# Kernel tuning notes

Measured on AMD Instinct MI355X. Metric: run time of the kernel, lower is better.

Reference implementation:

```python
import jax, jax.numpy as jnp
import numpy as np

INPUT_SIZE = 64
HIDDEN_SIZE = 128
LATENT_B = 8
BATCH = 512
SEQ = 2048


def setup_inputs() -> dict:
    key = jax.random.key(0)
    ks = jax.random.split(key, 8)
    s_fc = 1.0 / np.sqrt(INPUT_SIZE)
    s_gru = 1.0 / np.sqrt(LATENT_B)
    return {
        "latent_A_seq": jax.random.normal(ks[0], (BATCH, SEQ, INPUT_SIZE), dtype=jnp.float32),
        # fc_in: Linear(input_size -> hidden_size)
        "W_in": jax.random.uniform(ks[1], (HIDDEN_SIZE, INPUT_SIZE), jnp.float32, -s_fc, s_fc),
        "b_in": jax.random.uniform(ks[2], (HIDDEN_SIZE,), jnp.float32, -s_fc, s_fc),
        # GRU(hidden_size -> latent_dim_B), PyTorch layout: [3*H, in] stacked as (r, z, n)
        "W_ih": jax.random.uniform(ks[3], (3 * LATENT_B, HIDDEN_SIZE), jnp.float32, -s_gru, s_gru),
        "W_hh": jax.random.uniform(ks[4], (3 * LATENT_B, LATENT_B), jnp.float32, -s_gru, s_gru),
        "b_ih": jax.random.uniform(ks[5], (3 * LATENT_B,), jnp.float32, -s_gru, s_gru),
        "b_hh": jax.random.uniform(ks[6], (3 * LATENT_B,), jnp.float32, -s_gru, s_gru),
    }


def reference(latent_A_seq, W_in, b_in, W_ih, W_hh, b_ih, b_hh):
    # fc_in projection: (B, S, input) -> (B, S, hidden)
    x = jnp.einsum("bsi,hi->bsh", latent_A_seq, W_in) + b_in
    H = W_hh.shape[1]

    # Precompute input-side gate activations for all timesteps: (B, S, 3H)
    x_gates = jnp.einsum("bsh,gh->bsg", x, W_ih) + b_ih
    xr, xz, xn = jnp.split(x_gates, 3, axis=-1)

    Whr, Whz, Whn = jnp.split(W_hh, 3, axis=0)
    bhr, bhz, bhn = jnp.split(b_hh, 3, axis=0)

    def step(h, gates_t):
        xr_t, xz_t, xn_t = gates_t
        r = jax.nn.sigmoid(xr_t + h @ Whr.T + bhr)
        z = jax.nn.sigmoid(xz_t + h @ Whz.T + bhz)
        n = jnp.tanh(xn_t + r * (h @ Whn.T + bhn))
        h_new = (1.0 - z) * n + z * h
        return h_new, None

    h0 = jnp.zeros((latent_A_seq.shape[0], H), dtype=latent_A_seq.dtype)
    # scan over time: move seq axis to front -> (S, B, H) per gate
    seq_gates = (jnp.swapaxes(xr, 0, 1), jnp.swapaxes(xz, 0, 1), jnp.swapaxes(xn, 0, 1))
    h_final, _ = jax.lax.scan(step, h0, seq_gates)
    return h_final  # (B, latent_dim_B) == h_n.squeeze(0)
```

## Files before the change

### kernel.cpp

```cpp
#include <hip/hip_runtime.h>
#include <math.h>

#define BATCH  512
#define SEQ    2048
#define INPUT  64
#define HID    128
#define LB     8
#define NG     24
#define GSTRIDE (BATCH * NG)
#define T      16
#define NCHUNK (SEQ / T)
#define SLABF  (LB * NG)
#define CH_F   (T * SLABF)

__global__ void precompute_kernel(const float* __restrict__ W_in,
                                  const float* __restrict__ b_in,
                                  const float* __restrict__ W_ih,
                                  const float* __restrict__ b_ih,
                                  const float* __restrict__ b_hh,
                                  float* __restrict__ Wc,
                                  float* __restrict__ bc)
{
    int t = blockIdx.x * blockDim.x + threadIdx.x;
    if (t < NG * INPUT) {
        int g = t / INPUT, i = t % INPUT;
        float acc = 0.f;
        for (int h = 0; h < HID; ++h)
            acc += W_ih[g * HID + h] * W_in[h * INPUT + i];
        Wc[t] = acc;
    } else if (t < NG * INPUT + NG) {
        int g = t - NG * INPUT;
        float acc = b_ih[g];
        if (g < 2 * LB) acc += b_hh[g];
        for (int h = 0; h < HID; ++h)
            acc += W_ih[g * HID + h] * b_in[h];
        bc[g] = acc;
    }
}

#define TS 16
#define TB 8

__global__ __launch_bounds__(128) void gates_kernel(
    const float* __restrict__ A,
    const float* __restrict__ Wc,
    const float* __restrict__ bc,
    float* __restrict__ gates)
{
    const int s0 = blockIdx.x * TS;
    const int b0 = blockIdx.y * TB;
    const int tid = threadIdx.x;

    __shared__ float sA[TB * TS * 68];

#pragma unroll
    for (int it = 0; it < 16; ++it) {
        int f    = it * 128 + tid;
        int beta = f >> 8;
        int rem  = f & 255;
        int srow = rem >> 4;
        int c4   = rem & 15;
        float4 v = *(const float4*)(A + ((size_t)(b0 + beta) * SEQ + s0 + srow) * INPUT + c4 * 4);
        *(float4*)(&sA[(beta * TS + srow) * 68 + c4 * 4]) = v;
    }
    __syncthreads();

    const int bh = tid & 7;
    const int sh = tid >> 3;
    const float4* row4 = (const float4*)(&sA[(bh * TS + sh) * 68]);
    const float4* Wc4  = (const float4*)Wc;

    float acc[NG];
#pragma unroll
    for (int g = 0; g < NG; ++g) acc[g] = bc[g];

#pragma unroll
    for (int i = 0; i < 16; ++i) {
        float4 a = row4[i];
#pragma unroll
        for (int g = 0; g < NG; ++g) {
            float4 w = Wc4[g * 16 + i];
            acc[g] += a.x * w.x + a.y * w.y + a.z * w.z + a.w * w.w;
        }
    }

    float o[NG];
#pragma unroll
    for (int j = 0; j < LB; ++j) {
        o[j * 3 + 0] = acc[j];
        o[j * 3 + 1] = acc[8 + j];
        o[j * 3 + 2] = acc[16 + j];
    }
    float4* dst = (float4*)(gates + ((size_t)(s0 + sh) * BATCH + b0 + bh) * NG);
#pragma unroll
    for (int q = 0; q < 6; ++q)
        dst[q] = make_float4(o[4*q], o[4*q+1], o[4*q+2], o[4*q+3]);
}

#define ROR2(v)  __int_as_float(__builtin_amdgcn_update_dpp(0, __float_as_int(v), 0x122, 0xF, 0xF, false))
#define ROR4(v)  __int_as_float(__builtin_amdgcn_update_dpp(0, __float_as_int(v), 0x124, 0xF, 0xF, false))
#define ROR8(v)  __int_as_float(__builtin_amdgcn_update_dpp(0, __float_as_int(v), 0x128, 0xF, 0xF, false))

#define GATHER8(sl, x) do {      \
    sl[0] = (x);                 \
    sl[1] = ROR2(sl[0]);         \
    sl[2] = ROR4(sl[0]);         \
    sl[3] = ROR4(sl[1]);         \
    sl[4] = ROR8(sl[0]);         \
    sl[5] = ROR8(sl[1]);         \
    sl[6] = ROR8(sl[2]);         \
    sl[7] = ROR8(sl[3]);         \
} while (0)

__device__ __forceinline__ float dot8(const float* h, const float* w) {
    float d0 = fmaf(h[1], w[1], h[0] * w[0]);
    float d1 = fmaf(h[3], w[3], h[2] * w[2]);
    float d2 = fmaf(h[5], w[5], h[4] * w[4]);
    float d3 = fmaf(h[7], w[7], h[6] * w[6]);
    return (d0 + d1) + (d2 + d3);
}

__global__ __launch_bounds__(128) void scan_kernel(
    const float* __restrict__ gates,
    const float* __restrict__ W_hh,
    const float* __restrict__ b_hh,
    float* __restrict__ out)
{
    __shared__ float sbuf[2 * CH_F];
    const int tid = threadIdx.x;
    const int wv  = tid >> 6;
    const int l   = tid & 63;
    const int b0  = blockIdx.x * 8;

    if (wv == 1) {
        int off_g[12], off_l[12];
#pragma unroll
        for (int w = 0; w < 12; ++w) {
            int q  = w * 64 + l;
            int sw = q / 48;
            int rw = q - sw * 48;
            off_g[w] = sw * GSTRIDE + rw * 4;
            off_l[w] = sw * SLABF + rw * 4;
        }
        const float* gchunk = gates + (size_t)b0 * NG;

        float4 r[12];
#pragma unroll
        for (int w = 0; w < 12; ++w) r[w] = *(const float4*)(gchunk + off_g[w]);
        gchunk += (size_t)T * GSTRIDE;

        for (int c = 0; c < NCHUNK; ++c) {
            float* Ls = &sbuf[(c & 1) * CH_F];
#pragma unroll
            for (int w = 0; w < 12; ++w)
                *(float4*)(Ls + off_l[w]) = r[w];
            if (c + 1 < NCHUNK) {
#pragma unroll
                for (int w = 0; w < 12; ++w)
                    r[w] = *(const float4*)(gchunk + off_g[w]);
                gchunk += (size_t)T * GSTRIDE;
            }
            __syncthreads();
        }
        __syncthreads();
    } else {
        const int row = l >> 4;
        const int j   = (l >> 1) & 7;
        const int g   = l & 1;
        const int bh  = row * 2 + g;
        const int b   = b0 + bh;
        const int cofs = (bh * LB + j) * 3;

        float jdx[8];
        GATHER8(jdx, (float)j);
        float wr[8], wz[8], wn[8];
#pragma unroll
        for (int m = 0; m < 8; ++m) {
            int idx = (int)(jdx[m] + 0.5f);
            wr[m] = W_hh[(0 * LB + j) * LB + idx];
            wz[m] = W_hh[(1 * LB + j) * LB + idx];
            wn[m] = W_hh[(2 * LB + j) * LB + idx];
        }
        const float bhn = b_hh[2 * LB + j];

        float h = 0.f;
        __syncthreads();

        for (int c = 1; c <= NCHUNK; ++c) {
            const float* Lb = &sbuf[((c - 1) & 1) * CH_F] + cofs;

            float cr = Lb[0],         cz = Lb[1],         cn = Lb[2];
            float nr = Lb[SLABF + 0], nz = Lb[SLABF + 1], nn = Lb[SLABF + 2];
#pragma unroll
            for (int d = 0; d < T; ++d) {
                float fr = 0.f, fz = 0.f, fn = 0.f;
                if (d + 2 < T) {
                    const float* q = Lb + (d + 2) * SLABF;
                    fr = q[0]; fz = q[1]; fn = q[2];
                }

                float hs[8];
                GATHER8(hs, h);

                float dr = cr + dot8(hs, wr);
                float dz = cz + dot8(hs, wz);
                float dn = bhn + dot8(hs, wn);

                float rr = __builtin_amdgcn_rcpf(1.f + __expf(-dr));
                float zz = __builtin_amdgcn_rcpf(1.f + __expf(-dz));

                float t  = fmaf(rr, dn, cn);
                float nv = fmaf(-2.f, __builtin_amdgcn_rcpf(1.f + __expf(2.f * t)), 1.f);

                h = fmaf(zz, h - nv, nv);

                cr = nr; cz = nz; cn = nn;
                nr = fr; nz = fz; nn = fn;
            }
            __syncthreads();
        }

        out[b * LB + j] = h;
    }
}

extern "C" void kernel_launch(void* const* d_in, const int* in_sizes, int n_in,
                              void* d_out, int out_size, void* d_ws, size_t ws_size,
                              hipStream_t stream) {
    const float* A    = (const float*)d_in[0];
    const float* W_in = (const float*)d_in[1];
    const float* b_in = (const float*)d_in[2];
    const float* W_ih = (const float*)d_in[3];
    const float* W_hh = (const float*)d_in[4];
    const float* b_ih = (const float*)d_in[5];
    const float* b_hh = (const float*)d_in[6];
    float* out = (float*)d_out;

    float* gates = (float*)d_ws;
    float* Wc    = gates + (size_t)SEQ * BATCH * NG;
    float* bc    = Wc + NG * INPUT;

    precompute_kernel<<<7, 256, 0, stream>>>(W_in, b_in, W_ih, b_ih, b_hh, Wc, bc);

    dim3 ggrid(SEQ / TS, BATCH / TB);
    gates_kernel<<<ggrid, 128, 0, stream>>>(A, Wc, bc, gates);

    scan_kernel<<<BATCH / 8, 128, 0, stream>>>(gates, W_hh, b_hh, out);
}
```

Before: 723.9 us.

## Fuse gate projection into scan kernel with LDS-staged producer warps

Removes the separate gates kernel and its large global gate buffer. Three producer wavefronts per block now stream the input rows into LDS via global_load_lds with XOR swizzling and compute the gate slabs on the fly using packed v2f math, while one wavefront runs the recurrence. The log2e and sign scaling is folded into the weights and biases so the scan can call exp2 directly. This cuts global write and read traffic for the gates, but only 64 blocks of 256 threads run, so the overlap between the producer wavefronts and the serial scan decides whether the fused kernel keeps pace.

Result: faster. 701.2 us (-3.1%).

```diff
diff --git a/kernel.cpp b/kernel.cpp
--- a/kernel.cpp
+++ b/kernel.cpp
@@ -7,11 +7,24 @@
 #define HID    128
 #define LB     8
 #define NG     24
-#define GSTRIDE (BATCH * NG)
 #define T      16
 #define NCHUNK (SEQ / T)
 #define SLABF  (LB * NG)
 #define CH_F   (T * SLABF)
+#define ROWS   (T * LB)
+#define AF4C   (ROWS * 16)
+
+#define LOG2E  1.44269504088896340736f
+
+typedef float v2f __attribute__((ext_vector_type(2)));
+
+__device__ __forceinline__ v2f mk2(float a, float b) { v2f r; r.x = a; r.y = b; return r; }
+
+#if __has_builtin(__builtin_amdgcn_exp2f)
+#define EXP2F(x) __builtin_amdgcn_exp2f(x)
+#else
+#define EXP2F(x) __expf(0.69314718055994530942f * (x))
+#endif
 
 __global__ void precompute_kernel(const float* __restrict__ W_in,
                                   const float* __restrict__ b_in,
@@ -27,74 +40,17 @@
         float acc = 0.f;
         for (int h = 0; h < HID; ++h)
             acc += W_ih[g * HID + h] * W_in[h * INPUT + i];
-        Wc[t] = acc;
+        float sc = (g < 2 * LB) ? -LOG2E : 2.0f * LOG2E;
+        Wc[t] = acc * sc;
     } else if (t < NG * INPUT + NG) {
         int g = t - NG * INPUT;
         float acc = b_ih[g];
         if (g < 2 * LB) acc += b_hh[g];
         for (int h = 0; h < HID; ++h)
             acc += W_ih[g * HID + h] * b_in[h];
-        bc[g] = acc;
+        float sc = (g < 2 * LB) ? -LOG2E : 2.0f * LOG2E;
+        bc[g] = acc * sc;
     }
-}
-
-#define TS 16
-#define TB 8
-
-__global__ __launch_bounds__(128) void gates_kernel(
-    const float* __restrict__ A,
-    const float* __restrict__ Wc,
-    const float* __restrict__ bc,
-    float* __restrict__ gates)
-{
-    const int s0 = blockIdx.x * TS;
-    const int b0 = blockIdx.y * TB;
-    const int tid = threadIdx.x;
-
-    __shared__ float sA[TB * TS * 68];
-
-#pragma unroll
-    for (int it = 0; it < 16; ++it) {
-        int f    = it * 128 + tid;
-        int beta = f >> 8;
-        int rem  = f & 255;
-        int srow = rem >> 4;
-        int c4   = rem & 15;
-        float4 v = *(const float4*)(A + ((size_t)(b0 + beta) * SEQ + s0 + srow) * INPUT + c4 * 4);
-        *(float4*)(&sA[(beta * TS + srow) * 68 + c4 * 4]) = v;
-    }
-    __syncthreads();
-
-    const int bh = tid & 7;
-    const int sh = tid >> 3;
-    const float4* row4 = (const float4*)(&sA[(bh * TS + sh) * 68]);
-    const float4* Wc4  = (const float4*)Wc;
-
-    float acc[NG];
-#pragma unroll
-    for (int g = 0; g < NG; ++g) acc[g] = bc[g];
-
-#pragma unroll
-    for (int i = 0; i < 16; ++i) {
-        float4 a = row4[i];
-#pragma unroll
-        for (int g = 0; g < NG; ++g) {
-            float4 w = Wc4[g * 16 + i];
-            acc[g] += a.x * w.x + a.y * w.y + a.z * w.z + a.w * w.w;
-        }
-    }
-
-    float o[NG];
-#pragma unroll
-    for (int j = 0; j < LB; ++j) {
-        o[j * 3 + 0] = acc[j];
-        o[j * 3 + 1] = acc[8 + j];
-        o[j * 3 + 2] = acc[16 + j];
-    }
-    float4* dst = (float4*)(gates + ((size_t)(s0 + sh) * BATCH + b0 + bh) * NG);
-#pragma unroll
-    for (int q = 0; q < 6; ++q)
-        dst[q] = make_float4(o[4*q], o[4*q+1], o[4*q+2], o[4*q+3]);
 }
 
 #define ROR2(v)  __int_as_float(__builtin_amdgcn_update_dpp(0, __float_as_int(v), 0x122, 0xF, 0xF, false))
@@ -112,57 +68,104 @@
     sl[7] = ROR8(sl[3]);         \
 } while (0)
 
-__device__ __forceinline__ float dot8(const float* h, const float* w) {
-    float d0 = fmaf(h[1], w[1], h[0] * w[0]);
-    float d1 = fmaf(h[3], w[3], h[2] * w[2]);
-    float d2 = fmaf(h[5], w[5], h[4] * w[4]);
-    float d3 = fmaf(h[7], w[7], h[6] * w[6]);
-    return (d0 + d1) + (d2 + d3);
-}
-
-__global__ __launch_bounds__(128) void scan_kernel(
-    const float* __restrict__ gates,
+__global__ __launch_bounds__(256, 1) void fused_kernel(
+    const float* __restrict__ A,
+    const float* __restrict__ Wc,
+    const float* __restrict__ bc,
     const float* __restrict__ W_hh,
     const float* __restrict__ b_hh,
     float* __restrict__ out)
 {
-    __shared__ float sbuf[2 * CH_F];
+    __shared__ float4 abuf[2][AF4C];
+    __shared__ float  sbuf[2][CH_F];
+
     const int tid = threadIdx.x;
     const int wv  = tid >> 6;
     const int l   = tid & 63;
     const int b0  = blockIdx.x * 8;
 
-    if (wv == 1) {
-        int off_g[12], off_l[12];
-#pragma unroll
-        for (int w = 0; w < 12; ++w) {
-            int q  = w * 64 + l;
-            int sw = q / 48;
-            int rw = q - sw * 48;
-            off_g[w] = sw * GSTRIDE + rw * 4;
-            off_l[w] = sw * SLABF + rw * 4;
-        }
-        const float* gchunk = gates + (size_t)b0 * NG;
-
-        float4 r[12];
-#pragma unroll
-        for (int w = 0; w < 12; ++w) r[w] = *(const float4*)(gchunk + off_g[w]);
-        gchunk += (size_t)T * GSTRIDE;
-
-        for (int c = 0; c < NCHUNK; ++c) {
-            float* Ls = &sbuf[(c & 1) * CH_F];
-#pragma unroll
-            for (int w = 0; w < 12; ++w)
-                *(float4*)(Ls + off_l[w]) = r[w];
-            if (c + 1 < NCHUNK) {
-#pragma unroll
-                for (int w = 0; w < 12; ++w)
-                    r[w] = *(const float4*)(gchunk + off_g[w]);
-                gchunk += (size_t)T * GSTRIDE;
-            }
-            __syncthreads();
-        }
-        __syncthreads();
+    if (wv < 3) {
+        const int pg = wv * 64 + l;
+        const int gp = pg % 12;
+        const int rg = pg / 12;
+        const int g0 = gp * 2, g1 = g0 + 1;
+        const int j0 = g0 & 7, t0 = g0 >> 3;
+        const int j1 = g1 & 7, t1 = g1 >> 3;
+
+        v2f w0l[16], w0h[16], w1l[16], w1h[16];
+        const float4* W4 = (const float4*)Wc;
+#pragma unroll
+        for (int i = 0; i < 16; ++i) {
+            float4 a = W4[g0 * 16 + i];
+            float4 b = W4[g1 * 16 + i];
+            w0l[i] = mk2(a.x, a.y); w0h[i] = mk2(a.z, a.w);
+            w1l[i] = mk2(b.x, b.y); w1h[i] = mk2(b.z, b.w);
+        }
+        const float bc0 = bc[g0], bc1 = bc[g1];
+
+        auto stage = [&](int cc) {
+            float4* ab = &abuf[cc & 1][0];
+            const size_t srow = (size_t)cc * T;
+#pragma unroll
+            for (int k = 0; k < 11; ++k) {
+                int kk = k * 3 + wv;
+                if (kk < 32) {
+                    int q = kk * 64 + l;
+                    int r = q >> 4;
+                    int i = q & 15;
+                    int isrc = i ^ ((r >> 3) & 7);
+                    const float* gsrc = A
+                        + ((size_t)(b0 + (r >> 4)) * SEQ + srow + (size_t)(r & 15)) * INPUT
+                        + isrc * 4;
+                    __builtin_amdgcn_global_load_lds(
+                        (const __attribute__((address_space(1))) unsigned int*)gsrc,
+                        (__attribute__((address_space(3))) unsigned int*)(ab + kk * 64),
+                        16, 0, 0);
+                }
+            }
+        };
+
+        auto compute_slab = [&](int cc) {
+            const float4* ab = &abuf[cc & 1][0];
+            float* sl = &sbuf[cc & 1][0];
+#pragma unroll
+            for (int rit = 0; rit < 8; ++rit) {
+                const int r  = rg * 8 + rit;
+                const int xk = (r >> 3) & 7;
+                const float4* arow = ab + r * 16;
+                v2f acc0 = mk2(bc0, 0.f);
+                v2f acc1 = mk2(bc1, 0.f);
+#pragma unroll
+                for (int i = 0; i < 16; ++i) {
+                    float4 a4 = arow[i ^ xk];
+                    v2f alo = mk2(a4.x, a4.y);
+                    v2f ahi = mk2(a4.z, a4.w);
+                    acc0 = acc0 + alo * w0l[i] + ahi * w0h[i];
+                    acc1 = acc1 + alo * w1l[i] + ahi * w1h[i];
+                }
+                const int sw = r & 15, bh = r >> 4;
+                float* sp = sl + sw * SLABF + bh * (LB * 3);
+                sp[j0 * 3 + t0] = acc0.x + acc0.y;
+                sp[j1 * 3 + t1] = acc1.x + acc1.y;
+            }
+        };
+
+        stage(0);
+        asm volatile("s_waitcnt vmcnt(0)" ::: "memory");
+        __syncthreads();
+        stage(1);
+        compute_slab(0);
+        asm volatile("s_waitcnt vmcnt(0)" ::: "memory");
+        __syncthreads();
+
+        for (int p = 0; p < NCHUNK; ++p) {
+            if (p + 2 < NCHUNK) stage(p + 2);
+            if (p + 1 < NCHUNK) {
+                compute_slab(p + 1);
+                asm volatile("s_waitcnt vmcnt(0)" ::: "memory");
+                __syncthreads();
+            }
+        }
     } else {
         const int row = l >> 4;
         const int j   = (l >> 1) & 7;
@@ -171,23 +174,31 @@
         const int b   = b0 + bh;
         const int cofs = (bh * LB + j) * 3;
 
-        float jdx[8];
-        GATHER8(jdx, (float)j);
-        float wr[8], wz[8], wn[8];
+        float jdxv[8];
+        GATHER8(jdxv, (float)j);
+        float wrs[8], wzs[8], wns[8];
 #pragma unroll
         for (int m = 0; m < 8; ++m) {
-            int idx = (int)(jdx[m] + 0.5f);
-            wr[m] = W_hh[(0 * LB + j) * LB + idx];
-            wz[m] = W_hh[(1 * LB + j) * LB + idx];
-            wn[m] = W_hh[(2 * LB + j) * LB + idx];
-        }
-        const float bhn = b_hh[2 * LB + j];
+            int idx = (int)(jdxv[m] + 0.5f);
+            wrs[m] = W_hh[(0 * LB + j) * LB + idx] * (-LOG2E);
+            wzs[m] = W_hh[(1 * LB + j) * LB + idx] * (-LOG2E);
+            wns[m] = W_hh[(2 * LB + j) * LB + idx] * (2.0f * LOG2E);
+        }
+        v2f wr2[4], wz2[4], wn2[4];
+#pragma unroll
+        for (int m = 0; m < 4; ++m) {
+            wr2[m] = mk2(wrs[2 * m], wrs[2 * m + 1]);
+            wz2[m] = mk2(wzs[2 * m], wzs[2 * m + 1]);
+            wn2[m] = mk2(wns[2 * m], wns[2 * m + 1]);
+        }
+        const float bhn = b_hh[2 * LB + j] * (2.0f * LOG2E);
 
         float h = 0.f;
         __syncthreads();
-
-        for (int c = 1; c <= NCHUNK; ++c) {
-            const float* Lb = &sbuf[((c - 1) & 1) * CH_F] + cofs;
+        __syncthreads();
+
+        for (int p = 0; p < NCHUNK; ++p) {
+            const float* Lb = &sbuf[p & 1][cofs];
 
             float cr = Lb[0],         cz = Lb[1],         cn = Lb[2];
             float nr = Lb[SLABF + 0], nz = Lb[SLABF + 1], nn = Lb[SLABF + 2];
@@ -201,23 +212,34 @@
 
                 float hs[8];
                 GATHER8(hs, h);
-
-                float dr = cr + dot8(hs, wr);
-                float dz = cz + dot8(hs, wz);
-                float dn = bhn + dot8(hs, wn);
-
-                float rr = __builtin_amdgcn_rcpf(1.f + __expf(-dr));
-                float zz = __builtin_amdgcn_rcpf(1.f + __expf(-dz));
-
-                float t  = fmaf(rr, dn, cn);
-                float nv = fmaf(-2.f, __builtin_amdgcn_rcpf(1.f + __expf(2.f * t)), 1.f);
+                v2f h0 = mk2(hs[0], hs[1]);
+                v2f h1 = mk2(hs[2], hs[3]);
+                v2f h2 = mk2(hs[4], hs[5]);
+                v2f h3 = mk2(hs[6], hs[7]);
+
+                v2f srv = h0 * wr2[0] + h1 * wr2[1] + (h2 * wr2[2] + h3 * wr2[3]);
+                v2f szv = h0 * wz2[0] + h1 * wz2[1] + (h2 * wz2[2] + h3 * wz2[3]);
+                v2f snv = h0 * wn2[0] + h1 * wn2[1] + (h2 * wn2[2] + h3 * wn2[3]);
+
+                float dr = cr + (srv.x + srv.y);
+                float dz = cz + (szv.x + szv.y);
+                float dn = bhn + (snv.x + snv.y);
+
+                float er = EXP2F(dr);
+                float ez = EXP2F(dz);
+                float rr = __builtin_amdgcn_rcpf(1.f + er);
+                float zz = __builtin_amdgcn_rcpf(1.f + ez);
+
+                float tt = fmaf(rr, dn, cn);
+                float en = EXP2F(tt);
+                float nv = fmaf(-2.f, __builtin_amdgcn_rcpf(1.f + en), 1.f);
 
                 h = fmaf(zz, h - nv, nv);
 
                 cr = nr; cz = nz; cn = nn;
                 nr = fr; nz = fz; nn = fn;
             }
-            __syncthreads();
+            if (p + 1 < NCHUNK) __syncthreads();
         }
 
         out[b * LB + j] = h;
@@ -236,14 +258,9 @@
     const float* b_hh = (const float*)d_in[6];
     float* out = (float*)d_out;
 
-    float* gates = (float*)d_ws;
-    float* Wc    = gates + (size_t)SEQ * BATCH * NG;
-    float* bc    = Wc + NG * INPUT;
+    float* Wc = (float*)d_ws;
+    float* bc = Wc + NG * INPUT;
 
     precompute_kernel<<<7, 256, 0, stream>>>(W_in, b_in, W_ih, b_ih, b_hh, Wc, bc);
-
-    dim3 ggrid(SEQ / TS, BATCH / TB);
-    gates_kernel<<<ggrid, 128, 0, stream>>>(A, Wc, bc, gates);
-
-    scan_kernel<<<BATCH / 8, 128, 0, stream>>>(gates, W_hh, b_hh, out);
+    fused_kernel<<<BATCH / 8, 256, 0, stream>>>(A, Wc, bc, W_hh, b_hh, out);
 }
```
